# Optimization experiments

Measured on AMD Instinct MI355X. Metric: run time of the kernel, lower is better.

## Reference

```python
import jax, jax.numpy as jnp
import numpy as np

B, S, IN, OUT = 4, 512, 1024, 512
T, G, K, R = 16, 2, 4, 32  # tables, groups, cells, rank
OUTPUT_SCALE = 1.0 / np.sqrt(T * G).astype(np.float32)


def setup_inputs() -> dict:
    key = jax.random.key(0)
    k0, k1, k2, k3 = jax.random.split(key, 4)
    x = jax.random.normal(k0, (B, S, IN), dtype=jnp.float32)
    proj_w = jax.random.normal(k1, (R, IN), dtype=jnp.float32) / np.sqrt(IN)
    router_w = jax.random.normal(k2, (T, G, K, R), dtype=jnp.float32) / np.sqrt(R)
    router_b = jnp.zeros((T, G, K), dtype=jnp.float32)
    affine_w = jax.random.normal(k3, (T, G, K, R, OUT), dtype=jnp.float32) * 0.02
    affine_b = jnp.zeros((T, G, K, OUT), dtype=jnp.float32)
    return {"x": x, "proj_w": proj_w, "router_w": router_w, "router_b": router_b,
            "affine_w": affine_w, "affine_b": affine_b}


def reference(x, proj_w, router_w, router_b, affine_w, affine_b):
    # z: (B,S,R) low-rank projection
    z = jnp.einsum('bsi,ri->bsr', x, proj_w)
    # routing scores per (table, group, cell): (B,S,T,G,K)
    scores = jnp.einsum('bsr,tgkr->bstgk', z, router_w) + router_b
    # per-cell affine outputs: (B,S,T,G,K,O) -- dominant intermediate
    cell_values = jnp.einsum('bsr,tgkro->bstgko', z, affine_w) + affine_b
    # tropical (min-plus) winner selection: argmin over cells
    winner = jnp.argmin(scores, axis=-1)  # (B,S,T,G)
    idx = jnp.broadcast_to(winner[..., None, None],
                           winner.shape + (1, cell_values.shape[-1]))
    group_output = jnp.take_along_axis(cell_values, idx, axis=4)[..., 0, :]  # (B,S,T,G,O)
    # sum over groups then tables, apply output scaling
    output = group_output.sum(axis=(2, 3)) * OUTPUT_SCALE  # (B,S,O)
    return output
```

## Files before the change

kernel.cpp:

```cpp
#include <hip/hip_runtime.h>

#define NTOK 2048
#define IN_DIM 1024
#define OUT_DIM 512
#define RNK 32
#define TG_N 32
#define TGK_N 128
#define AWCOLS 4096
#define KD 4224
#define NKT 66
#define SCALE_F 0.17677669529663687f

typedef __attribute__((ext_vector_type(8))) short short8;
typedef __attribute__((ext_vector_type(4))) float float4v;

__device__ __forceinline__ unsigned short f2bf(float f) {
  union { float f; unsigned int u; } c; c.f = f;
  unsigned int u = c.u;
  u += 0x7fffu + ((u >> 16) & 1u);
  return (unsigned short)(u >> 16);
}

__global__ __launch_bounds__(256) void k_w2t(
    const float* __restrict__ aw, const float* __restrict__ ab,
    unsigned short* __restrict__ w2t) {
  __shared__ float tile[32][33];
  const int c0 = blockIdx.x * 32, o0 = blockIdx.y * 32;
  const int t = threadIdx.x;
  const int oo = t & 31, cc = t >> 5;
#pragma unroll
  for (int p = 0; p < 4; ++p) {
    int cidx = c0 + cc + p * 8;
    float v = (cidx < AWCOLS)
                  ? aw[(size_t)cidx * OUT_DIM + o0 + oo]
                  : ab[(size_t)(cidx - AWCOLS) * OUT_DIM + o0 + oo];
    tile[cc + p * 8][oo] = v;
  }
  __syncthreads();
  if (t < 128) {
    const int ol = t >> 2, ch = t & 3;
    union { short8 v; unsigned short u[8]; } pk;
#pragma unroll
    for (int j = 0; j < 8; ++j) pk.u[j] = f2bf(tile[ch * 8 + j][ol]);
    *(short8*)(w2t + (size_t)(o0 + ol) * KD + c0 + ch * 8) = pk.v;
  }
}

__global__ __launch_bounds__(256) void k_zwin(
    const float* __restrict__ x, const float* __restrict__ proj_w,
    const float* __restrict__ router_w, const float* __restrict__ router_b,
    unsigned short* __restrict__ zout, unsigned long long* __restrict__ wout) {
  const int tok2 = blockIdx.x * 2;
  const int t = threadIdx.x;
  __shared__ __align__(16) float zbuf[2][RNK];
  __shared__ float sc[2][TGK_N];
  __shared__ int winbuf[2][TG_N];

  const int r = t >> 3, c = t & 7;
  const float4* w4 = (const float4*)(proj_w + (size_t)r * IN_DIM);
  const float4* x0 = (const float4*)(x + (size_t)tok2 * IN_DIM);
  float a0 = 0.f, a1 = 0.f;
#pragma unroll
  for (int jj = 0; jj < 32; ++jj) {
    float4 wv = w4[jj * 8 + c];
    float4 xv0 = x0[jj * 8 + c];
    float4 xv1 = x0[256 + jj * 8 + c];
    a0 += xv0.x * wv.x + xv0.y * wv.y + xv0.z * wv.z + xv0.w * wv.w;
    a1 += xv1.x * wv.x + xv1.y * wv.y + xv1.z * wv.z + xv1.w * wv.w;
  }
  a0 += __shfl_xor(a0, 1); a0 += __shfl_xor(a0, 2); a0 += __shfl_xor(a0, 4);
  a1 += __shfl_xor(a1, 1); a1 += __shfl_xor(a1, 2); a1 += __shfl_xor(a1, 4);
  if (c == 0) { zbuf[0][r] = a0; zbuf[1][r] = a1; }
  __syncthreads();

  {
    const int cell = t & 127, tk = t >> 7;
    const float4* rw = (const float4*)(router_w + (size_t)cell * RNK);
    const float4* zb = (const float4*)(&zbuf[tk][0]);
    float s = router_b[cell];
#pragma unroll
    for (int j = 0; j < 8; ++j) {
      float4 a = rw[j]; float4 b = zb[j];
      s += a.x * b.x + a.y * b.y + a.z * b.z + a.w * b.w;
    }
    sc[tk][cell] = s;
  }
  __syncthreads();

  if (t < 64) {
    const int tk = t >> 5, tg = t & 31;
    float best = sc[tk][tg * 4]; int w = 0;
#pragma unroll
    for (int k = 1; k < 4; ++k) {
      float v = sc[tk][tg * 4 + k];
      if (v < best) { best = v; w = k; }
    }
    winbuf[tk][tg] = w;
    zout[(size_t)(tok2 + tk) * RNK + tg] = f2bf(zbuf[tk][tg]);
  }
  __syncthreads();
  if (t < 2) {
    unsigned long long w = 0ull;
    for (int g = 0; g < TG_N; ++g)
      w |= ((unsigned long long)(winbuf[t][g] & 3)) << (2 * g);
    wout[tok2 + t] = w;
  }
}

__global__ __launch_bounds__(256) void k_gemm(
    const unsigned short* __restrict__ z, const unsigned long long* __restrict__ win,
    const unsigned short* __restrict__ Bt, float* __restrict__ out) {
  __shared__ __align__(16) unsigned short Bs[8][2048];
  const int bm = blockIdx.x, bn = blockIdx.y;
  const int tid = threadIdx.x;
  const int wave = tid >> 6, lane = tid & 63;
  const int l15 = lane & 15, quad = lane >> 4;
  const int mw = (wave & 1) * 32;
  const int nw = (wave >> 1) * 16;

  const int m0 = bm * 64 + mw + l15;
  const int m1 = m0 + 16;
  short8 z0 = *(const short8*)(z + (size_t)m0 * RNK + quad * 8);
  short8 z1 = *(const short8*)(z + (size_t)m1 * RNK + quad * 8);
  const unsigned long long w0 = win[m0], w1 = win[m1];

  const int sn = tid >> 3;
  const unsigned short* bsrc =
      Bt + (size_t)(bn * 32 + sn) * KD + (((tid & 7) ^ (sn & 7)) * 8);

  const int fn = nw + l15;
  float4v acc0 = {}, acc1 = {};

#define ISSUE(KT)                                                              \
  __builtin_amdgcn_global_load_lds(                                            \
      (const __attribute__((address_space(1))) void*)(bsrc + (size_t)(KT) * 64), \
      (__attribute__((address_space(3))) void*)(&Bs[(KT) & 7][wave * 512]),    \
      16, 0, 0)

  auto compute = [&](int kt) __attribute__((always_inline)) {
    const unsigned short* sb = &Bs[kt & 7][0];
    if (kt < 64) {
      const int tg = kt >> 1;
      const unsigned e0 = (unsigned)(w0 >> (2 * tg)) & 3u;
      const unsigned e1 = (unsigned)(w1 >> (2 * tg)) & 3u;
#pragma unroll
      for (int s = 0; s < 2; ++s) {
        const unsigned kk = (unsigned)(((kt & 1) << 1) | s);
        short8 zz = {};
        short8 b = *(const short8*)(sb + fn * 64 + (((s * 4 + quad) ^ (fn & 7)) * 8));
        acc0 = __builtin_amdgcn_mfma_f32_16x16x32_bf16(e0 == kk ? z0 : zz, b, acc0, 0, 0, 0);
        acc1 = __builtin_amdgcn_mfma_f32_16x16x32_bf16(e1 == kk ? z1 : zz, b, acc1, 0, 0, 0);
      }
    } else {
#pragma unroll
      for (int s = 0; s < 2; ++s) {
        const int tgA = (kt - 64) * 16 + s * 8 + quad * 2;
        union { short8 v; unsigned long long q[2]; } fa, fb;
        fa.q[0] = 0x3F80ull << (((unsigned)(w0 >> (2 * tgA)) & 3u) * 16);
        fa.q[1] = 0x3F80ull << (((unsigned)(w0 >> (2 * (tgA + 1))) & 3u) * 16);
        fb.q[0] = 0x3F80ull << (((unsigned)(w1 >> (2 * tgA)) & 3u) * 16);
        fb.q[1] = 0x3F80ull << (((unsigned)(w1 >> (2 * (tgA + 1))) & 3u) * 16);
        short8 b = *(const short8*)(sb + fn * 64 + (((s * 4 + quad) ^ (fn & 7)) * 8));
        acc0 = __builtin_amdgcn_mfma_f32_16x16x32_bf16(fa.v, b, acc0, 0, 0, 0);
        acc1 = __builtin_amdgcn_mfma_f32_16x16x32_bf16(fb.v, b, acc1, 0, 0, 0);
      }
    }
  };

  ISSUE(0); ISSUE(1); ISSUE(2); ISSUE(3); ISSUE(4); ISSUE(5); ISSUE(6);

  for (int kt = 0; kt < 60; ++kt) {
    asm volatile("s_waitcnt vmcnt(6)" ::: "memory");
    asm volatile("s_barrier" ::: "memory");
    if (kt <= 58) ISSUE(kt + 7);
    compute(kt);
  }
  asm volatile("s_waitcnt vmcnt(5)" ::: "memory"); asm volatile("s_barrier" ::: "memory"); compute(60);
  asm volatile("s_waitcnt vmcnt(4)" ::: "memory"); asm volatile("s_barrier" ::: "memory"); compute(61);
  asm volatile("s_waitcnt vmcnt(3)" ::: "memory"); asm volatile("s_barrier" ::: "memory"); compute(62);
  asm volatile("s_waitcnt vmcnt(2)" ::: "memory"); asm volatile("s_barrier" ::: "memory"); compute(63);
  asm volatile("s_waitcnt vmcnt(1)" ::: "memory"); asm volatile("s_barrier" ::: "memory"); compute(64);
  asm volatile("s_waitcnt vmcnt(0)" ::: "memory"); asm volatile("s_barrier" ::: "memory"); compute(65);
#undef ISSUE

  const int col = bn * 32 + nw + l15;
#pragma unroll
  for (int tm = 0; tm < 2; ++tm) {
    float4v a = tm ? acc1 : acc0;
    const int rowb = bm * 64 + mw + tm * 16 + quad * 4;
#pragma unroll
    for (int rg = 0; rg < 4; ++rg)
      out[(size_t)(rowb + rg) * OUT_DIM + col] = a[rg] * SCALE_F;
  }
}

extern "C" void kernel_launch(void* const* d_in, const int* in_sizes, int n_in,
                              void* d_out, int out_size, void* d_ws, size_t ws_size,
                              hipStream_t stream) {
  const float* x        = (const float*)d_in[0];
  const float* proj_w   = (const float*)d_in[1];
  const float* router_w = (const float*)d_in[2];
  const float* router_b = (const float*)d_in[3];
  const float* affine_w = (const float*)d_in[4];
  const float* affine_b = (const float*)d_in[5];
  float* out = (float*)d_out;

  unsigned short* zout = (unsigned short*)d_ws;
  unsigned long long* wout = (unsigned long long*)((char*)d_ws + 131072);
  unsigned short* w2t = (unsigned short*)((char*)d_ws + 147456);

  k_w2t<<<dim3(KD / 32, OUT_DIM / 32), 256, 0, stream>>>(affine_w, affine_b, w2t);
  k_zwin<<<NTOK / 2, 256, 0, stream>>>(x, proj_w, router_w, router_b, zout, wout);
  k_gemm<<<dim3(NTOK / 64, OUT_DIM / 32), 256, 0, stream>>>(zout, wout, w2t, out);
}
```

Measured before the change: 106.5 us.

## Merge prep kernels and split GEMM K across waves with direct register loads

The weight-transpose kernel and the z/winner kernel are merged into one launch whose block index picks the role, removing a kernel launch and letting both jobs run at once. The GEMM drops the LDS-staged async pipeline. Each block now covers a smaller 32x16 output tile, the four waves split the K dimension, and each wave loads B fragments straight from global into registers with a two-step prefetch. Partial sums are then reduced through shared memory. This yields more blocks and less barrier cost, but each wave reuses B less, so global read traffic rises, and the reduction adds an epilogue.

```diff
diff --git a/kernel.cpp b/kernel.cpp
--- a/kernel.cpp
+++ b/kernel.cpp
@@ -10,6 +10,7 @@
 #define KD 4224
 #define NKT 66
 #define SCALE_F 0.17677669529663687f
+#define W2T_BLOCKS 2112
 
 typedef __attribute__((ext_vector_type(8))) short short8;
 typedef __attribute__((ext_vector_type(4))) float float4v;
@@ -21,46 +22,46 @@
   return (unsigned short)(u >> 16);
 }
 
-__global__ __launch_bounds__(256) void k_w2t(
+__global__ __launch_bounds__(256, 4) void k_prep(
     const float* __restrict__ aw, const float* __restrict__ ab,
-    unsigned short* __restrict__ w2t) {
-  __shared__ float tile[32][33];
-  const int c0 = blockIdx.x * 32, o0 = blockIdx.y * 32;
-  const int t = threadIdx.x;
-  const int oo = t & 31, cc = t >> 5;
-#pragma unroll
-  for (int p = 0; p < 4; ++p) {
-    int cidx = c0 + cc + p * 8;
-    float v = (cidx < AWCOLS)
-                  ? aw[(size_t)cidx * OUT_DIM + o0 + oo]
-                  : ab[(size_t)(cidx - AWCOLS) * OUT_DIM + o0 + oo];
-    tile[cc + p * 8][oo] = v;
-  }
-  __syncthreads();
-  if (t < 128) {
-    const int ol = t >> 2, ch = t & 3;
-    union { short8 v; unsigned short u[8]; } pk;
-#pragma unroll
-    for (int j = 0; j < 8; ++j) pk.u[j] = f2bf(tile[ch * 8 + j][ol]);
-    *(short8*)(w2t + (size_t)(o0 + ol) * KD + c0 + ch * 8) = pk.v;
-  }
-}
-
-__global__ __launch_bounds__(256) void k_zwin(
     const float* __restrict__ x, const float* __restrict__ proj_w,
     const float* __restrict__ router_w, const float* __restrict__ router_b,
+    unsigned short* __restrict__ w2t,
     unsigned short* __restrict__ zout, unsigned long long* __restrict__ wout) {
-  const int tok2 = blockIdx.x * 2;
   const int t = threadIdx.x;
+
+  if (blockIdx.x < W2T_BLOCKS) {
+    __shared__ float tile[32][33];
+    const int c0 = (blockIdx.x % 132) * 32, o0 = (blockIdx.x / 132) * 32;
+    const int oo = t & 31, cc = t >> 5;
+#pragma unroll
+    for (int p = 0; p < 4; ++p) {
+      int cidx = c0 + cc + p * 8;
+      float v = (cidx < AWCOLS)
+                    ? aw[(size_t)cidx * OUT_DIM + o0 + oo]
+                    : ab[(size_t)(cidx - AWCOLS) * OUT_DIM + o0 + oo];
+      tile[cc + p * 8][oo] = v;
+    }
+    __syncthreads();
+    if (t < 128) {
+      const int ol = t >> 2, ch = t & 3;
+      union { short8 v; unsigned short u[8]; } pk;
+#pragma unroll
+      for (int j = 0; j < 8; ++j) pk.u[j] = f2bf(tile[ch * 8 + j][ol]);
+      *(short8*)(w2t + (size_t)(o0 + ol) * KD + c0 + ch * 8) = pk.v;
+    }
+    return;
+  }
+
   __shared__ __align__(16) float zbuf[2][RNK];
   __shared__ float sc[2][TGK_N];
   __shared__ int winbuf[2][TG_N];
-
+  const int tok2 = (blockIdx.x - W2T_BLOCKS) * 2;
   const int r = t >> 3, c = t & 7;
   const float4* w4 = (const float4*)(proj_w + (size_t)r * IN_DIM);
   const float4* x0 = (const float4*)(x + (size_t)tok2 * IN_DIM);
   float a0 = 0.f, a1 = 0.f;
-#pragma unroll
+#pragma unroll 8
   for (int jj = 0; jj < 32; ++jj) {
     float4 wv = w4[jj * 8 + c];
     float4 xv0 = x0[jj * 8 + c];
@@ -107,50 +108,36 @@
   }
 }
 
-__global__ __launch_bounds__(256) void k_gemm(
+__global__ __launch_bounds__(256, 4) void k_gemm(
     const unsigned short* __restrict__ z, const unsigned long long* __restrict__ win,
     const unsigned short* __restrict__ Bt, float* __restrict__ out) {
-  __shared__ __align__(16) unsigned short Bs[8][2048];
+  __shared__ float red[3][512];
   const int bm = blockIdx.x, bn = blockIdx.y;
   const int tid = threadIdx.x;
   const int wave = tid >> 6, lane = tid & 63;
   const int l15 = lane & 15, quad = lane >> 4;
-  const int mw = (wave & 1) * 32;
-  const int nw = (wave >> 1) * 16;
-
-  const int m0 = bm * 64 + mw + l15;
+
+  const int m0 = bm * 32 + l15;
   const int m1 = m0 + 16;
   short8 z0 = *(const short8*)(z + (size_t)m0 * RNK + quad * 8);
   short8 z1 = *(const short8*)(z + (size_t)m1 * RNK + quad * 8);
   const unsigned long long w0 = win[m0], w1 = win[m1];
 
-  const int sn = tid >> 3;
-  const unsigned short* bsrc =
-      Bt + (size_t)(bn * 32 + sn) * KD + (((tid & 7) ^ (sn & 7)) * 8);
-
-  const int fn = nw + l15;
+  const unsigned short* bp = Bt + (size_t)(bn * 16 + l15) * KD + quad * 8;
+
   float4v acc0 = {}, acc1 = {};
 
-#define ISSUE(KT)                                                              \
-  __builtin_amdgcn_global_load_lds(                                            \
-      (const __attribute__((address_space(1))) void*)(bsrc + (size_t)(KT) * 64), \
-      (__attribute__((address_space(3))) void*)(&Bs[(KT) & 7][wave * 512]),    \
-      16, 0, 0)
-
-  auto compute = [&](int kt) __attribute__((always_inline)) {
-    const unsigned short* sb = &Bs[kt & 7][0];
+  auto compute = [&](int kt, short8 ba, short8 bb) __attribute__((always_inline)) {
     if (kt < 64) {
       const int tg = kt >> 1;
       const unsigned e0 = (unsigned)(w0 >> (2 * tg)) & 3u;
       const unsigned e1 = (unsigned)(w1 >> (2 * tg)) & 3u;
-#pragma unroll
-      for (int s = 0; s < 2; ++s) {
-        const unsigned kk = (unsigned)(((kt & 1) << 1) | s);
-        short8 zz = {};
-        short8 b = *(const short8*)(sb + fn * 64 + (((s * 4 + quad) ^ (fn & 7)) * 8));
-        acc0 = __builtin_amdgcn_mfma_f32_16x16x32_bf16(e0 == kk ? z0 : zz, b, acc0, 0, 0, 0);
-        acc1 = __builtin_amdgcn_mfma_f32_16x16x32_bf16(e1 == kk ? z1 : zz, b, acc1, 0, 0, 0);
-      }
+      const unsigned kk0 = (unsigned)((kt & 1) << 1), kk1 = kk0 | 1u;
+      short8 zz = {};
+      acc0 = __builtin_amdgcn_mfma_f32_16x16x32_bf16(e0 == kk0 ? z0 : zz, ba, acc0, 0, 0, 0);
+      acc1 = __builtin_amdgcn_mfma_f32_16x16x32_bf16(e1 == kk0 ? z1 : zz, ba, acc1, 0, 0, 0);
+      acc0 = __builtin_amdgcn_mfma_f32_16x16x32_bf16(e0 == kk1 ? z0 : zz, bb, acc0, 0, 0, 0);
+      acc1 = __builtin_amdgcn_mfma_f32_16x16x32_bf16(e1 == kk1 ? z1 : zz, bb, acc1, 0, 0, 0);
     } else {
 #pragma unroll
       for (int s = 0; s < 2; ++s) {
@@ -160,37 +147,53 @@
         fa.q[1] = 0x3F80ull << (((unsigned)(w0 >> (2 * (tgA + 1))) & 3u) * 16);
         fb.q[0] = 0x3F80ull << (((unsigned)(w1 >> (2 * tgA)) & 3u) * 16);
         fb.q[1] = 0x3F80ull << (((unsigned)(w1 >> (2 * (tgA + 1))) & 3u) * 16);
-        short8 b = *(const short8*)(sb + fn * 64 + (((s * 4 + quad) ^ (fn & 7)) * 8));
+        short8 b = s ? bb : ba;
         acc0 = __builtin_amdgcn_mfma_f32_16x16x32_bf16(fa.v, b, acc0, 0, 0, 0);
         acc1 = __builtin_amdgcn_mfma_f32_16x16x32_bf16(fb.v, b, acc1, 0, 0, 0);
       }
     }
   };
 
-  ISSUE(0); ISSUE(1); ISSUE(2); ISSUE(3); ISSUE(4); ISSUE(5); ISSUE(6);
-
-  for (int kt = 0; kt < 60; ++kt) {
-    asm volatile("s_waitcnt vmcnt(6)" ::: "memory");
-    asm volatile("s_barrier" ::: "memory");
-    if (kt <= 58) ISSUE(kt + 7);
-    compute(kt);
-  }
-  asm volatile("s_waitcnt vmcnt(5)" ::: "memory"); asm volatile("s_barrier" ::: "memory"); compute(60);
-  asm volatile("s_waitcnt vmcnt(4)" ::: "memory"); asm volatile("s_barrier" ::: "memory"); compute(61);
-  asm volatile("s_waitcnt vmcnt(3)" ::: "memory"); asm volatile("s_barrier" ::: "memory"); compute(62);
-  asm volatile("s_waitcnt vmcnt(2)" ::: "memory"); asm volatile("s_barrier" ::: "memory"); compute(63);
-  asm volatile("s_waitcnt vmcnt(1)" ::: "memory"); asm volatile("s_barrier" ::: "memory"); compute(64);
-  asm volatile("s_waitcnt vmcnt(0)" ::: "memory"); asm volatile("s_barrier" ::: "memory"); compute(65);
-#undef ISSUE
-
-  const int col = bn * 32 + nw + l15;
-#pragma unroll
-  for (int tm = 0; tm < 2; ++tm) {
-    float4v a = tm ? acc1 : acc0;
-    const int rowb = bm * 64 + mw + tm * 16 + quad * 4;
-#pragma unroll
-    for (int rg = 0; rg < 4; ++rg)
-      out[(size_t)(rowb + rg) * OUT_DIM + col] = a[rg] * SCALE_F;
+  const int klo = (wave < 2) ? wave * 17 : 34 + (wave - 2) * 16;
+  const int khi = klo + ((wave < 2) ? 17 : 16);
+
+  short8 b0a = *(const short8*)(bp + (size_t)klo * 64);
+  short8 b0b = *(const short8*)(bp + (size_t)klo * 64 + 32);
+  short8 b1a = *(const short8*)(bp + (size_t)(klo + 1) * 64);
+  short8 b1b = *(const short8*)(bp + (size_t)(klo + 1) * 64 + 32);
+
+#pragma unroll 2
+  for (int kt = klo; kt < khi; ++kt) {
+    const int kf = (kt + 2 < khi) ? kt + 2 : khi - 1;
+    short8 pa = *(const short8*)(bp + (size_t)kf * 64);
+    short8 pb = *(const short8*)(bp + (size_t)kf * 64 + 32);
+    compute(kt, b0a, b0b);
+    b0a = b1a; b0b = b1b; b1a = pa; b1b = pb;
+  }
+
+  if (wave > 0) {
+#pragma unroll
+    for (int j = 0; j < 4; ++j) {
+      red[wave - 1][j * 64 + lane] = acc0[j];
+      red[wave - 1][(j + 4) * 64 + lane] = acc1[j];
+    }
+  }
+  __syncthreads();
+  if (wave == 0) {
+#pragma unroll
+    for (int j = 0; j < 4; ++j) {
+      acc0[j] += red[0][j * 64 + lane] + red[1][j * 64 + lane] + red[2][j * 64 + lane];
+      acc1[j] += red[0][(j + 4) * 64 + lane] + red[1][(j + 4) * 64 + lane] + red[2][(j + 4) * 64 + lane];
+    }
+    const int col = bn * 16 + l15;
+#pragma unroll
+    for (int tm = 0; tm < 2; ++tm) {
+      float4v a = tm ? acc1 : acc0;
+      const int rowb = bm * 32 + tm * 16 + quad * 4;
+#pragma unroll
+      for (int rg = 0; rg < 4; ++rg)
+        out[(size_t)(rowb + rg) * OUT_DIM + col] = a[rg] * SCALE_F;
+    }
   }
 }
 
@@ -209,7 +212,7 @@
   unsigned long long* wout = (unsigned long long*)((char*)d_ws + 131072);
   unsigned short* w2t = (unsigned short*)((char*)d_ws + 147456);
 
-  k_w2t<<<dim3(KD / 32, OUT_DIM / 32), 256, 0, stream>>>(affine_w, affine_b, w2t);
-  k_zwin<<<NTOK / 2, 256, 0, stream>>>(x, proj_w, router_w, router_b, zout, wout);
-  k_gemm<<<dim3(NTOK / 64, OUT_DIM / 32), 256, 0, stream>>>(zout, wout, w2t, out);
-}
+  k_prep<<<W2T_BLOCKS + NTOK / 2, 256, 0, stream>>>(
+      affine_w, affine_b, x, proj_w, router_w, router_b, w2t, zout, wout);
+  k_gemm<<<dim3(NTOK / 32, OUT_DIM / 16), 256, 0, stream>>>(zout, wout, w2t, out);
+}
```

Result: slower. 133.1 us (+25.0%).

## Enlarge GEMM M-tile to 128 rows and remap blocks for XCD-aware B reuse

Applied to the files above, without the earlier changes.

Each GEMM block now covers 128 token rows by 32 output columns, with every wave computing a 32x32 sub-tile (four accumulators) instead of a 32x16 one. This halves the number of blocks that stream each B column-tile from global memory and doubles the MFMA work per LDS B fragment. A 1D grid of 256 blocks is remapped so that blocks on the same XCD (blk & 7) share bn values, aiming to improve L2 reuse of the B slabs. The trade-off is fewer blocks (256 rather than 512) on a GPU with many CUs, which lowers occupancy and latency hiding.

```diff
diff --git a/kernel.cpp b/kernel.cpp
--- a/kernel.cpp
+++ b/kernel.cpp
@@ -111,14 +111,15 @@
     const unsigned short* __restrict__ z, const unsigned long long* __restrict__ win,
     const unsigned short* __restrict__ Bt, float* __restrict__ out) {
   __shared__ __align__(16) unsigned short Bs[8][2048];
-  const int bm = blockIdx.x, bn = blockIdx.y;
+  const int blk = blockIdx.x;
+  const int g = blk & 7, rest = blk >> 3;
+  const int bn = g * 2 + (rest & 1);
+  const int bm = rest >> 1;
   const int tid = threadIdx.x;
   const int wave = tid >> 6, lane = tid & 63;
   const int l15 = lane & 15, quad = lane >> 4;
-  const int mw = (wave & 1) * 32;
-  const int nw = (wave >> 1) * 16;
-
-  const int m0 = bm * 64 + mw + l15;
+
+  const int m0 = bm * 128 + wave * 32 + l15;
   const int m1 = m0 + 16;
   short8 z0 = *(const short8*)(z + (size_t)m0 * RNK + quad * 8);
   short8 z1 = *(const short8*)(z + (size_t)m1 * RNK + quad * 8);
@@ -128,17 +129,17 @@
   const unsigned short* bsrc =
       Bt + (size_t)(bn * 32 + sn) * KD + (((tid & 7) ^ (sn & 7)) * 8);
 
-  const int fn = nw + l15;
-  float4v acc0 = {}, acc1 = {};
-
-#define ISSUE(KT)                                                              \
-  __builtin_amdgcn_global_load_lds(                                            \
+  float4v acc00 = {}, acc01 = {}, acc10 = {}, acc11 = {};
+
+#define ISSUE(KT)                                                                \
+  __builtin_amdgcn_global_load_lds(                                              \
       (const __attribute__((address_space(1))) void*)(bsrc + (size_t)(KT) * 64), \
-      (__attribute__((address_space(3))) void*)(&Bs[(KT) & 7][wave * 512]),    \
+      (__attribute__((address_space(3))) void*)(&Bs[(KT) & 7][wave * 512]),      \
       16, 0, 0)
 
   auto compute = [&](int kt) __attribute__((always_inline)) {
     const unsigned short* sb = &Bs[kt & 7][0];
+    const int fn0 = l15, fn1 = 16 + l15;
     if (kt < 64) {
       const int tg = kt >> 1;
       const unsigned e0 = (unsigned)(w0 >> (2 * tg)) & 3u;
@@ -147,9 +148,14 @@
       for (int s = 0; s < 2; ++s) {
         const unsigned kk = (unsigned)(((kt & 1) << 1) | s);
         short8 zz = {};
-        short8 b = *(const short8*)(sb + fn * 64 + (((s * 4 + quad) ^ (fn & 7)) * 8));
-        acc0 = __builtin_amdgcn_mfma_f32_16x16x32_bf16(e0 == kk ? z0 : zz, b, acc0, 0, 0, 0);
-        acc1 = __builtin_amdgcn_mfma_f32_16x16x32_bf16(e1 == kk ? z1 : zz, b, acc1, 0, 0, 0);
+        short8 a0 = (e0 == kk) ? z0 : zz;
+        short8 a1 = (e1 == kk) ? z1 : zz;
+        short8 b0 = *(const short8*)(sb + fn0 * 64 + (((s * 4 + quad) ^ (fn0 & 7)) * 8));
+        short8 b1 = *(const short8*)(sb + fn1 * 64 + (((s * 4 + quad) ^ (fn1 & 7)) * 8));
+        acc00 = __builtin_amdgcn_mfma_f32_16x16x32_bf16(a0, b0, acc00, 0, 0, 0);
+        acc01 = __builtin_amdgcn_mfma_f32_16x16x32_bf16(a0, b1, acc01, 0, 0, 0);
+        acc10 = __builtin_amdgcn_mfma_f32_16x16x32_bf16(a1, b0, acc10, 0, 0, 0);
+        acc11 = __builtin_amdgcn_mfma_f32_16x16x32_bf16(a1, b1, acc11, 0, 0, 0);
       }
     } else {
 #pragma unroll
@@ -160,9 +166,12 @@
         fa.q[1] = 0x3F80ull << (((unsigned)(w0 >> (2 * (tgA + 1))) & 3u) * 16);
         fb.q[0] = 0x3F80ull << (((unsigned)(w1 >> (2 * tgA)) & 3u) * 16);
         fb.q[1] = 0x3F80ull << (((unsigned)(w1 >> (2 * (tgA + 1))) & 3u) * 16);
-        short8 b = *(const short8*)(sb + fn * 64 + (((s * 4 + quad) ^ (fn & 7)) * 8));
-        acc0 = __builtin_amdgcn_mfma_f32_16x16x32_bf16(fa.v, b, acc0, 0, 0, 0);
-        acc1 = __builtin_amdgcn_mfma_f32_16x16x32_bf16(fb.v, b, acc1, 0, 0, 0);
+        short8 b0 = *(const short8*)(sb + fn0 * 64 + (((s * 4 + quad) ^ (fn0 & 7)) * 8));
+        short8 b1 = *(const short8*)(sb + fn1 * 64 + (((s * 4 + quad) ^ (fn1 & 7)) * 8));
+        acc00 = __builtin_amdgcn_mfma_f32_16x16x32_bf16(fa.v, b0, acc00, 0, 0, 0);
+        acc01 = __builtin_amdgcn_mfma_f32_16x16x32_bf16(fa.v, b1, acc01, 0, 0, 0);
+        acc10 = __builtin_amdgcn_mfma_f32_16x16x32_bf16(fb.v, b0, acc10, 0, 0, 0);
+        acc11 = __builtin_amdgcn_mfma_f32_16x16x32_bf16(fb.v, b1, acc11, 0, 0, 0);
       }
     }
   };
@@ -183,14 +192,17 @@
   asm volatile("s_waitcnt vmcnt(0)" ::: "memory"); asm volatile("s_barrier" ::: "memory"); compute(65);
 #undef ISSUE
 
-  const int col = bn * 32 + nw + l15;
 #pragma unroll
   for (int tm = 0; tm < 2; ++tm) {
-    float4v a = tm ? acc1 : acc0;
-    const int rowb = bm * 64 + mw + tm * 16 + quad * 4;
-#pragma unroll
-    for (int rg = 0; rg < 4; ++rg)
-      out[(size_t)(rowb + rg) * OUT_DIM + col] = a[rg] * SCALE_F;
+#pragma unroll
+    for (int tn = 0; tn < 2; ++tn) {
+      float4v a = tm ? (tn ? acc11 : acc10) : (tn ? acc01 : acc00);
+      const int col = bn * 32 + tn * 16 + l15;
+      const int rowb = bm * 128 + wave * 32 + tm * 16 + quad * 4;
+#pragma unroll
+      for (int rg = 0; rg < 4; ++rg)
+        out[(size_t)(rowb + rg) * OUT_DIM + col] = a[rg] * SCALE_F;
+    }
   }
 }
 
@@ -211,5 +223,5 @@
 
   k_w2t<<<dim3(KD / 32, OUT_DIM / 32), 256, 0, stream>>>(affine_w, affine_b, w2t);
   k_zwin<<<NTOK / 2, 256, 0, stream>>>(x, proj_w, router_w, router_b, zout, wout);
-  k_gemm<<<dim3(NTOK / 64, OUT_DIM / 32), 256, 0, stream>>>(zout, wout, w2t, out);
-}
+  k_gemm<<<256, 256, 0, stream>>>(zout, wout, w2t, out);
+}
```

Result: no change. 108.3 us (+1.6%).
